# Kernel tuning notes

Hardware: AMD Instinct MI355X
Metric: run time of the kernel (lower is better)

Reference implementation:

```python
import jax, jax.numpy as jnp
import numpy as np

EMBED = 512
HEADS = 8
INTER = 512
HEAD_DIM = INTER // HEADS
ROPE_BASE = 10000.0


def rot_half(x):
    x1 = x[..., ::2]
    x2 = x[..., 1::2]
    return jnp.stack([-x2, x1], axis=-1).reshape(x.shape)


def apply_rope(x, cos, sin):
    # cos/sin: (1, T, 1, 1, D//2) -> repeat-interleave to D
    cos = jnp.repeat(cos, 2, axis=-1)
    sin = jnp.repeat(sin, 2, axis=-1)
    return x * cos + rot_half(x) * sin


def setup_inputs() -> dict:
    key = jax.random.key(0)
    ks = jax.random.split(key, 8)
    B, T, P, E = 2, 512, 16, EMBED
    s_in = 1.0 / np.sqrt(E)
    x = jax.random.normal(ks[0], (B, T, P, E), dtype=jnp.float32)
    q_w = jax.random.normal(ks[1], (INTER, E), dtype=jnp.float32) * s_in
    k_w = jax.random.normal(ks[2], (INTER, E), dtype=jnp.float32) * s_in
    v_w = jax.random.normal(ks[3], (INTER, E), dtype=jnp.float32) * s_in
    q_b = jax.random.normal(ks[4], (INTER,), dtype=jnp.float32) * 0.01
    k_b = jax.random.normal(ks[5], (INTER,), dtype=jnp.float32) * 0.01
    v_b = jax.random.normal(ks[6], (INTER,), dtype=jnp.float32) * 0.01
    proj_w = jax.random.normal(ks[7], (E, INTER), dtype=jnp.float32) * (1.0 / np.sqrt(INTER))
    return {"x": x, "q_w": q_w, "q_b": q_b, "k_w": k_w, "k_b": k_b,
            "v_w": v_w, "v_b": v_b, "proj_w": proj_w}


def reference(x, q_w, q_b, k_w, k_b, v_w, v_b, proj_w):
    B, T, P, E = x.shape
    H, D = HEADS, HEAD_DIM
    q = (x @ q_w.T + q_b).reshape(B, T, P, H, D)
    k = (x @ k_w.T + k_b).reshape(B, T, P, H, D)
    v = (x @ v_w.T + v_b).reshape(B, T, P, H, D)
    # RoPE cache over time axis
    inv_freq = 1.0 / (ROPE_BASE ** (jnp.arange(0, D, 2, dtype=jnp.float32) / D))
    freqs = jnp.arange(T, dtype=jnp.float32)[:, None] * inv_freq[None, :]  # (T, D//2)
    cos_t = jnp.cos(freqs).reshape(1, T, 1, 1, D // 2)
    sin_t = jnp.sin(freqs).reshape(1, T, 1, 1, D // 2)
    q = apply_rope(q, cos_t, sin_t)
    k = apply_rope(k, cos_t, sin_t)
    scale = D ** (-0.5)
    scores = jnp.einsum('btphd,buphd->bphtu', q, k) * scale  # (B,P,H,T,T)
    causal_mask = jnp.triu(jnp.ones((T, T), dtype=bool), k=1)
    scores = jnp.where(causal_mask, -jnp.inf, scores)
    probs = jax.nn.softmax(scores, axis=-1)
    y = jnp.einsum('bphtu,buphd->btphd', probs, v).reshape(B, T, P, H * D)
    return y @ proj_w.T
```

## Files before the change

kernel.cpp:

```cpp
#include <hip/hip_runtime.h>
#include <hip/hip_bf16.h>
#include <math.h>

typedef __bf16 bf16x8 __attribute__((ext_vector_type(8)));
typedef float f32x4 __attribute__((ext_vector_type(4)));
typedef unsigned short u16;

#define MROWS 16384
#define TT 512
#define PP 16

__device__ __forceinline__ u16 f2bf(float f) {
    union { float f; unsigned int i; } v; v.f = f;
    unsigned int x = v.i;
    return (u16)((x + 0x7FFFu + ((x >> 16) & 1u)) >> 16);
}

__device__ __forceinline__ void async16(const u16* g, u16* lds) {
    __builtin_amdgcn_global_load_lds(
        (const __attribute__((address_space(1))) void*)g,
        (__attribute__((address_space(3))) void*)lds, 16, 0, 0);
}

__global__ __launch_bounds__(256) void cvt_k(const float* __restrict__ s,
                                             u16* __restrict__ d) {
    long i = (long)blockIdx.x * 256 + threadIdx.x;
    const float4* p = (const float4*)s + i * 2;
    float4 a = p[0], b = p[1];
    u16 t[8] = { f2bf(a.x), f2bf(a.y), f2bf(a.z), f2bf(a.w),
                 f2bf(b.x), f2bf(b.y), f2bf(b.z), f2bf(b.w) };
    *(uint4*)(d + i * 8) = *(const uint4*)t;
}

__global__ __launch_bounds__(256) void cvtw_k(const float* __restrict__ q,
                                              const float* __restrict__ k,
                                              const float* __restrict__ v,
                                              const float* __restrict__ pw,
                                              u16* __restrict__ d) {
    int m = blockIdx.y;
    const float* s = (m == 0) ? q : (m == 1) ? k : (m == 2) ? v : pw;
    long i = (long)blockIdx.x * 256 + threadIdx.x;
    const float4* p = (const float4*)s + i * 2;
    float4 a = p[0], b = p[1];
    u16 t[8] = { f2bf(a.x), f2bf(a.y), f2bf(a.z), f2bf(a.w),
                 f2bf(b.x), f2bf(b.y), f2bf(b.z), f2bf(b.w) };
    *(uint4*)(d + (long)m * 262144 + i * 8) = *(const uint4*)t;
}

template<bool QKV>
__global__ __launch_bounds__(256, 2)
void gemm_k(const u16* __restrict__ A, const u16* __restrict__ Wall,
            const float* __restrict__ bq, const float* __restrict__ bk,
            const float* __restrict__ bv,
            u16* __restrict__ Oq, u16* __restrict__ Ok, u16* __restrict__ Ov,
            float* __restrict__ Of)
{
    __shared__ u16 As[128 * 64];
    __shared__ u16 Bs[128 * 64];

    const int tid  = threadIdx.x;
    const int wv   = tid >> 6;
    const int lane = tid & 63;
    const int quad = lane >> 4;
    const int l16  = lane & 15;
    const int wm   = wv >> 1, wn = wv & 1;

    const int blockM = blockIdx.x;
    const int blockN = blockIdx.y;

    const u16* W; const float* bias; u16* OutB; int ncol0; int section = 0;
    if constexpr (QKV) {
        section = blockN >> 2;
        ncol0 = (blockN & 3) * 128;
        W    = Wall + (long)section * 262144;
        bias = (section == 0) ? bq : (section == 1) ? bk : bv;
        OutB = (section == 0) ? Oq : (section == 1) ? Ok : Ov;
    } else {
        ncol0 = blockN * 128;
        W = Wall; bias = nullptr; OutB = nullptr;
    }

    const int gm0 = blockM * 128;
    const int lr  = lane >> 3;
    const int lc  = (lane & 7) ^ lr;

    f32x4 acc[4][4] = {};

    for (int kk = 0; kk < 8; ++kk) {
        const int k0 = kk * 64;
        __syncthreads();
        #pragma unroll
        for (int i = 0; i < 4; ++i) {
            const int rb = wv * 32 + i * 8;
            async16(&A[(long)(gm0   + rb + lr) * 512 + k0 + lc * 8], &As[rb * 64]);
            async16(&W[(long)(ncol0 + rb + lr) * 512 + k0 + lc * 8], &Bs[rb * 64]);
        }
        __syncthreads();

        #pragma unroll
        for (int ks = 0; ks < 2; ++ks) {
            bf16x8 af[4], bf_[4];
            #pragma unroll
            for (int ms = 0; ms < 4; ++ms) {
                const int R = wm * 64 + ms * 16 + l16;
                af[ms] = *(const bf16x8*)&As[(R * 8 + ((ks * 4 + quad) ^ (l16 & 7))) * 8];
            }
            #pragma unroll
            for (int ns = 0; ns < 4; ++ns) {
                const int R = wn * 64 + ns * 16 + l16;
                bf_[ns] = *(const bf16x8*)&Bs[(R * 8 + ((ks * 4 + quad) ^ (l16 & 7))) * 8];
            }
            #pragma unroll
            for (int ms = 0; ms < 4; ++ms)
                #pragma unroll
                for (int ns = 0; ns < 4; ++ns)
                    acc[ms][ns] = __builtin_amdgcn_mfma_f32_16x16x32_bf16(af[ms], bf_[ns], acc[ms][ns], 0, 0, 0);
        }
    }

    #pragma unroll
    for (int ms = 0; ms < 4; ++ms) {
        const int g_m0 = gm0 + wm * 64 + ms * 16 + quad * 4;
        #pragma unroll
        for (int ns = 0; ns < 4; ++ns) {
            const int n_local = ncol0 + wn * 64 + ns * 16 + l16;
            float bval = 0.f;
            if constexpr (QKV) bval = bias[n_local];
            #pragma unroll
            for (int r = 0; r < 4; ++r) {
                float val = acc[ms][ns][r] + bval;
                const size_t off = (size_t)(g_m0 + r) * 512 + n_local;
                if constexpr (QKV) {
                    float partner = __shfl_xor(val, 1, 64);
                    if (section < 2) {
                        const int m = g_m0 + r;
                        const int t = (m >> 4) & 511;
                        const int d = n_local & 63;
                        float ang = (float)t * __expf(-(float)(d & ~1) * (9.210340371976184f / 64.0f));
                        float s_, c_;
                        __sincosf(ang, &s_, &c_);
                        val = (d & 1) ? (val * c_ + partner * s_)
                                      : (val * c_ - partner * s_);
                    }
                    OutB[off] = f2bf(val);
                } else {
                    Of[off] = val;
                }
            }
        }
    }
}

__global__ __launch_bounds__(256, 4)
void attn_k(const u16* __restrict__ Q, const u16* __restrict__ K,
            const u16* __restrict__ V, u16* __restrict__ Y)
{
    __shared__ u16 Sh[64 * 64];
    __shared__ u16 Vt[64][72];

    const int tid  = threadIdx.x;
    const int wv   = tid >> 6;
    const int lane = tid & 63;
    const int quad = lane >> 4;
    const int l16  = lane & 15;
    const int lr   = lane >> 3;
    const int lc   = (lane & 7) ^ lr;

    const int pairx = blockIdx.x;
    const int hid = blockIdx.y;
    const int b = hid >> 7;
    const int p = (hid >> 3) & 15;
    const int h = hid & 7;

    const int base = ((b * TT) * PP + p) * 512 + h * 64;
    const int rowStride = PP * 512;

    for (int sel = 0; sel < 2; ++sel) {
        const int qt = sel ? (7 - pairx) : pairx;
        const int t0 = qt * 64;

        __syncthreads();
        #pragma unroll
        for (int i = 0; i < 2; ++i) {
            const int rb = wv * 16 + i * 8;
            async16(&Q[base + (t0 + rb + lr) * rowStride + lc * 8], &Sh[rb * 64]);
        }
        __syncthreads();
        bf16x8 qf[2];
        {
            const int R = wv * 16 + l16;
            #pragma unroll
            for (int ks = 0; ks < 2; ++ks)
                qf[ks] = *(const bf16x8*)&Sh[(R * 8 + ((ks * 4 + quad) ^ (l16 & 7))) * 8];
        }

        float m_i[4], l_i[4], alpha[4];
        f32x4 o[4] = {};
        #pragma unroll
        for (int j = 0; j < 4; ++j) { m_i[j] = -3.0e38f; l_i[j] = 0.f; }

        for (int ui = 0; ui <= qt; ++ui) {
            const int u0 = ui * 64;
            __syncthreads();
            #pragma unroll
            for (int i = 0; i < 2; ++i) {
                const int rb = wv * 16 + i * 8;
                async16(&K[base + (u0 + rb + lr) * rowStride + lc * 8], &Sh[rb * 64]);
            }
            #pragma unroll
            for (int i = 0; i < 4; ++i) {
                int task = tid + i * 256;
                int u = task >> 4, dc = (task & 15) * 4;
                uint2 vvv = *(const uint2*)&V[base + (u0 + u) * rowStride + dc];
                Vt[dc + 0][u] = (u16)(vvv.x & 0xFFFF);
                Vt[dc + 1][u] = (u16)(vvv.x >> 16);
                Vt[dc + 2][u] = (u16)(vvv.y & 0xFFFF);
                Vt[dc + 3][u] = (u16)(vvv.y >> 16);
            }
            __syncthreads();

            f32x4 s[4] = {};
            #pragma unroll
            for (int ks = 0; ks < 2; ++ks) {
                bf16x8 bk_[4];
                #pragma unroll
                for (int ns = 0; ns < 4; ++ns) {
                    const int R = ns * 16 + l16;
                    bk_[ns] = *(const bf16x8*)&Sh[(R * 8 + ((ks * 4 + quad) ^ (l16 & 7))) * 8];
                }
                #pragma unroll
                for (int ns = 0; ns < 4; ++ns)
                    s[ns] = __builtin_amdgcn_mfma_f32_16x16x32_bf16(qf[ks], bk_[ns], s[ns], 0, 0, 0);
            }
            __syncthreads();

            if (ui == qt) {
                #pragma unroll
                for (int ns = 0; ns < 4; ++ns)
                    #pragma unroll
                    for (int r = 0; r < 4; ++r) {
                        int trow = wv * 16 + quad * 4 + r;
                        int ucol = ns * 16 + l16;
                        float v = s[ns][r] * 0.125f;
                        s[ns][r] = (ucol > trow) ? -1.0e30f : v;
                    }
            } else {
                #pragma unroll
                for (int ns = 0; ns < 4; ++ns)
                    #pragma unroll
                    for (int r = 0; r < 4; ++r)
                        s[ns][r] *= 0.125f;
            }
            #pragma unroll
            for (int r = 0; r < 4; ++r) {
                float tmax = s[0][r];
                #pragma unroll
                for (int ns = 1; ns < 4; ++ns) tmax = fmaxf(tmax, s[ns][r]);
                #pragma unroll
                for (int off = 1; off < 16; off <<= 1)
                    tmax = fmaxf(tmax, __shfl_xor(tmax, off, 64));
                float mn = fmaxf(m_i[r], tmax);
                alpha[r] = __expf(fminf(m_i[r] - mn, 0.f));
                m_i[r] = mn;
                float rsum = 0.f;
                #pragma unroll
                for (int ns = 0; ns < 4; ++ns) {
                    float e = __expf(fminf(s[ns][r] - mn, 0.f));
                    s[ns][r] = e;
                    rsum += e;
                }
                #pragma unroll
                for (int off = 1; off < 16; off <<= 1)
                    rsum += __shfl_xor(rsum, off, 64);
                l_i[r] = l_i[r] * alpha[r] + rsum;
            }
            #pragma unroll
            for (int nd = 0; nd < 4; ++nd)
                #pragma unroll
                for (int r = 0; r < 4; ++r)
                    o[nd][r] *= alpha[r];
            #pragma unroll
            for (int ns = 0; ns < 4; ++ns)
                #pragma unroll
                for (int r = 0; r < 4; ++r) {
                    const int row = wv * 16 + quad * 4 + r;
                    const int cu  = ns * 2 + (l16 >> 3);
                    Sh[(row * 8 + (cu ^ (row & 7))) * 8 + (l16 & 7)] = f2bf(s[ns][r]);
                }
            __syncthreads();
            #pragma unroll
            for (int ks = 0; ks < 2; ++ks) {
                const int R = wv * 16 + l16;
                bf16x8 ap = *(const bf16x8*)&Sh[(R * 8 + ((ks * 4 + quad) ^ (l16 & 7))) * 8];
                bf16x8 bv_[4];
                #pragma unroll
                for (int nd = 0; nd < 4; ++nd)
                    bv_[nd] = *(const bf16x8*)&Vt[nd * 16 + l16][ks * 32 + quad * 8];
                #pragma unroll
                for (int nd = 0; nd < 4; ++nd)
                    o[nd] = __builtin_amdgcn_mfma_f32_16x16x32_bf16(ap, bv_[nd], o[nd], 0, 0, 0);
            }
        }

        #pragma unroll
        for (int nd = 0; nd < 4; ++nd)
            #pragma unroll
            for (int r = 0; r < 4; ++r) {
                int t = t0 + wv * 16 + quad * 4 + r;
                int d = nd * 16 + l16;
                float val = o[nd][r] / l_i[r];
                int ym = (b * TT + t) * PP + p;
                Y[ym * 512 + h * 64 + d] = f2bf(val);
            }
    }
}

extern "C" void kernel_launch(void* const* d_in, const int* in_sizes, int n_in,
                              void* d_out, int out_size, void* d_ws, size_t ws_size,
                              hipStream_t stream) {
    const float* x  = (const float*)d_in[0];
    const float* qw = (const float*)d_in[1];
    const float* qb = (const float*)d_in[2];
    const float* kw = (const float*)d_in[3];
    const float* kb = (const float*)d_in[4];
    const float* vw = (const float*)d_in[5];
    const float* vb = (const float*)d_in[6];
    const float* pw = (const float*)d_in[7];

    u16* ws   = (u16*)d_ws;
    u16* xb   = ws;
    u16* wAll = ws + (size_t)MROWS * 512;
    u16* Qb   = wAll + 4 * 262144;
    u16* Vb   = (u16*)d_out;
    u16* Kb   = (u16*)d_out + (size_t)MROWS * 512;

    cvt_k<<<4096, 256, 0, stream>>>(x, xb);
    cvtw_k<<<dim3(128, 4), 256, 0, stream>>>(qw, kw, vw, pw, wAll);
    gemm_k<true><<<dim3(128, 12), 256, 0, stream>>>(xb, wAll, qb, kb, vb,
                                                    Qb, Kb, Vb, nullptr);
    attn_k<<<dim3(4, 256), 256, 0, stream>>>(Qb, Kb, Vb, Qb);
    gemm_k<false><<<dim3(128, 4), 256, 0, stream>>>(Qb, wAll + 3 * 262144,
                                                    nullptr, nullptr, nullptr,
                                                    nullptr, nullptr, nullptr,
                                                    (float*)d_out);
}
```

Measured before the change: 195.9 us.

## Pre-transpose V, fold softmax scale into Q, compute row sums via MFMA

Adds a separate kernel that writes V transposed per head plane, so attention can async-load V tiles into swizzled LDS. The block no longer transposes V in LDS every iteration. The softmax scale and log2e are folded into Q at the projection epilogue so exp2f can be used directly. Row sums are accumulated with an extra MFMA against a ones vector instead of shuffle reductions. Blocks now handle one query tile each, with separate K, V and P LDS buffers and higher occupancy. The cost is an extra kernel launch and a round trip through global memory.

```diff
diff --git a/kernel.cpp b/kernel.cpp
--- a/kernel.cpp
+++ b/kernel.cpp
@@ -141,6 +141,7 @@
                         __sincosf(ang, &s_, &c_);
                         val = (d & 1) ? (val * c_ + partner * s_)
                                       : (val * c_ - partner * s_);
+                        if (section == 0) val *= 0.18033688011112042f;
                     }
                     OutB[off] = f2bf(val);
                 } else {
@@ -151,12 +152,41 @@
     }
 }
 
-__global__ __launch_bounds__(256, 4)
+__global__ __launch_bounds__(256) void tv_k(const u16* __restrict__ Vb,
+                                            u16* __restrict__ Vtg) {
+    __shared__ u16 Vs[64][72];
+    const int tid = threadIdx.x;
+    const int ut = blockIdx.x, plane = blockIdx.y;
+    const int b = plane >> 7, p = (plane >> 3) & 15, h = plane & 7;
+    const int base = ((b * TT) * PP + p) * 512 + h * 64;
+    const int u0 = ut * 64;
+    #pragma unroll
+    for (int i = 0; i < 4; ++i) {
+        int task = tid + i * 256;
+        int u = task >> 4, dc = (task & 15) * 4;
+        uint2 vv = *(const uint2*)&Vb[base + (u0 + u) * 8192 + dc];
+        Vs[dc + 0][u] = (u16)(vv.x & 0xFFFF);
+        Vs[dc + 1][u] = (u16)(vv.x >> 16);
+        Vs[dc + 2][u] = (u16)(vv.y & 0xFFFF);
+        Vs[dc + 3][u] = (u16)(vv.y >> 16);
+    }
+    __syncthreads();
+    #pragma unroll
+    for (int i = 0; i < 2; ++i) {
+        int task = tid + i * 256;
+        int d = task >> 3, uc = (task & 7) * 8;
+        *(uint4*)&Vtg[(size_t)plane * 32768 + d * 512 + u0 + uc] =
+            *(const uint4*)&Vs[d][uc];
+    }
+}
+
+__global__ __launch_bounds__(256, 6)
 void attn_k(const u16* __restrict__ Q, const u16* __restrict__ K,
-            const u16* __restrict__ V, u16* __restrict__ Y)
+            const u16* __restrict__ Vtg, u16* __restrict__ Y)
 {
-    __shared__ u16 Sh[64 * 64];
-    __shared__ u16 Vt[64][72];
+    __shared__ u16 ShK[64 * 64];
+    __shared__ u16 ShV[64 * 64];
+    __shared__ u16 ShP[64 * 64];
 
     const int tid  = threadIdx.x;
     const int wv   = tid >> 6;
@@ -166,7 +196,8 @@
     const int lr   = lane >> 3;
     const int lc   = (lane & 7) ^ lr;
 
-    const int pairx = blockIdx.x;
+    const int qt  = 7 - blockIdx.x;
+    const int t0  = qt * 64;
     const int hid = blockIdx.y;
     const int b = hid >> 7;
     const int p = (hid >> 3) & 15;
@@ -174,145 +205,125 @@
 
     const int base = ((b * TT) * PP + p) * 512 + h * 64;
     const int rowStride = PP * 512;
-
-    for (int sel = 0; sel < 2; ++sel) {
-        const int qt = sel ? (7 - pairx) : pairx;
-        const int t0 = qt * 64;
-
+    const size_t planeOff = (size_t)hid * 32768;
+
+    #pragma unroll
+    for (int i = 0; i < 2; ++i) {
+        const int rb = wv * 16 + i * 8;
+        async16(&Q[base + (t0 + rb + lr) * rowStride + lc * 8], &ShK[rb * 64]);
+    }
+    __syncthreads();
+    bf16x8 qf[2];
+    {
+        const int R = wv * 16 + l16;
+        #pragma unroll
+        for (int ks = 0; ks < 2; ++ks)
+            qf[ks] = *(const bf16x8*)&ShK[(R * 8 + ((ks * 4 + quad) ^ (l16 & 7))) * 8];
+    }
+
+    bf16x8 ones;
+    #pragma unroll
+    for (int j = 0; j < 8; ++j) ones[j] = (__bf16)1.0f;
+
+    float m_i[4], alpha[4];
+    f32x4 o[4] = {};
+    f32x4 ol = {};
+    #pragma unroll
+    for (int j = 0; j < 4; ++j) m_i[j] = -3.0e38f;
+
+    for (int ui = 0; ui <= qt; ++ui) {
+        const int u0 = ui * 64;
         __syncthreads();
         #pragma unroll
         for (int i = 0; i < 2; ++i) {
             const int rb = wv * 16 + i * 8;
-            async16(&Q[base + (t0 + rb + lr) * rowStride + lc * 8], &Sh[rb * 64]);
-        }
-        __syncthreads();
-        bf16x8 qf[2];
-        {
-            const int R = wv * 16 + l16;
-            #pragma unroll
-            for (int ks = 0; ks < 2; ++ks)
-                qf[ks] = *(const bf16x8*)&Sh[(R * 8 + ((ks * 4 + quad) ^ (l16 & 7))) * 8];
-        }
-
-        float m_i[4], l_i[4], alpha[4];
-        f32x4 o[4] = {};
-        #pragma unroll
-        for (int j = 0; j < 4; ++j) { m_i[j] = -3.0e38f; l_i[j] = 0.f; }
-
-        for (int ui = 0; ui <= qt; ++ui) {
-            const int u0 = ui * 64;
-            __syncthreads();
-            #pragma unroll
-            for (int i = 0; i < 2; ++i) {
-                const int rb = wv * 16 + i * 8;
-                async16(&K[base + (u0 + rb + lr) * rowStride + lc * 8], &Sh[rb * 64]);
-            }
-            #pragma unroll
-            for (int i = 0; i < 4; ++i) {
-                int task = tid + i * 256;
-                int u = task >> 4, dc = (task & 15) * 4;
-                uint2 vvv = *(const uint2*)&V[base + (u0 + u) * rowStride + dc];
-                Vt[dc + 0][u] = (u16)(vvv.x & 0xFFFF);
-                Vt[dc + 1][u] = (u16)(vvv.x >> 16);
-                Vt[dc + 2][u] = (u16)(vvv.y & 0xFFFF);
-                Vt[dc + 3][u] = (u16)(vvv.y >> 16);
-            }
-            __syncthreads();
-
-            f32x4 s[4] = {};
-            #pragma unroll
-            for (int ks = 0; ks < 2; ++ks) {
-                bf16x8 bk_[4];
-                #pragma unroll
-                for (int ns = 0; ns < 4; ++ns) {
-                    const int R = ns * 16 + l16;
-                    bk_[ns] = *(const bf16x8*)&Sh[(R * 8 + ((ks * 4 + quad) ^ (l16 & 7))) * 8];
-                }
-                #pragma unroll
-                for (int ns = 0; ns < 4; ++ns)
-                    s[ns] = __builtin_amdgcn_mfma_f32_16x16x32_bf16(qf[ks], bk_[ns], s[ns], 0, 0, 0);
-            }
-            __syncthreads();
-
-            if (ui == qt) {
-                #pragma unroll
-                for (int ns = 0; ns < 4; ++ns)
-                    #pragma unroll
-                    for (int r = 0; r < 4; ++r) {
-                        int trow = wv * 16 + quad * 4 + r;
-                        int ucol = ns * 16 + l16;
-                        float v = s[ns][r] * 0.125f;
-                        s[ns][r] = (ucol > trow) ? -1.0e30f : v;
-                    }
-            } else {
-                #pragma unroll
-                for (int ns = 0; ns < 4; ++ns)
-                    #pragma unroll
-                    for (int r = 0; r < 4; ++r)
-                        s[ns][r] *= 0.125f;
-            }
-            #pragma unroll
-            for (int r = 0; r < 4; ++r) {
-                float tmax = s[0][r];
-                #pragma unroll
-                for (int ns = 1; ns < 4; ++ns) tmax = fmaxf(tmax, s[ns][r]);
-                #pragma unroll
-                for (int off = 1; off < 16; off <<= 1)
-                    tmax = fmaxf(tmax, __shfl_xor(tmax, off, 64));
-                float mn = fmaxf(m_i[r], tmax);
-                alpha[r] = __expf(fminf(m_i[r] - mn, 0.f));
-                m_i[r] = mn;
-                float rsum = 0.f;
-                #pragma unroll
-                for (int ns = 0; ns < 4; ++ns) {
-                    float e = __expf(fminf(s[ns][r] - mn, 0.f));
-                    s[ns][r] = e;
-                    rsum += e;
-                }
-                #pragma unroll
-                for (int off = 1; off < 16; off <<= 1)
-                    rsum += __shfl_xor(rsum, off, 64);
-                l_i[r] = l_i[r] * alpha[r] + rsum;
-            }
-            #pragma unroll
-            for (int nd = 0; nd < 4; ++nd)
-                #pragma unroll
-                for (int r = 0; r < 4; ++r)
-                    o[nd][r] *= alpha[r];
+            async16(&K[base + (u0 + rb + lr) * rowStride + lc * 8], &ShK[rb * 64]);
+            async16(&Vtg[planeOff + (rb + lr) * 512 + u0 + lc * 8], &ShV[rb * 64]);
+        }
+        __syncthreads();
+
+        f32x4 s[4] = {};
+        #pragma unroll
+        for (int ks = 0; ks < 2; ++ks) {
+            bf16x8 bk_[4];
+            #pragma unroll
+            for (int ns = 0; ns < 4; ++ns) {
+                const int R = ns * 16 + l16;
+                bk_[ns] = *(const bf16x8*)&ShK[(R * 8 + ((ks * 4 + quad) ^ (l16 & 7))) * 8];
+            }
+            #pragma unroll
+            for (int ns = 0; ns < 4; ++ns)
+                s[ns] = __builtin_amdgcn_mfma_f32_16x16x32_bf16(qf[ks], bk_[ns], s[ns], 0, 0, 0);
+        }
+
+        if (ui == qt) {
             #pragma unroll
             for (int ns = 0; ns < 4; ++ns)
                 #pragma unroll
                 for (int r = 0; r < 4; ++r) {
-                    const int row = wv * 16 + quad * 4 + r;
-                    const int cu  = ns * 2 + (l16 >> 3);
-                    Sh[(row * 8 + (cu ^ (row & 7))) * 8 + (l16 & 7)] = f2bf(s[ns][r]);
+                    int trow = wv * 16 + quad * 4 + r;
+                    int ucol = ns * 16 + l16;
+                    if (ucol > trow) s[ns][r] = -1.0e30f;
                 }
-            __syncthreads();
-            #pragma unroll
-            for (int ks = 0; ks < 2; ++ks) {
-                const int R = wv * 16 + l16;
-                bf16x8 ap = *(const bf16x8*)&Sh[(R * 8 + ((ks * 4 + quad) ^ (l16 & 7))) * 8];
-                bf16x8 bv_[4];
-                #pragma unroll
-                for (int nd = 0; nd < 4; ++nd)
-                    bv_[nd] = *(const bf16x8*)&Vt[nd * 16 + l16][ks * 32 + quad * 8];
-                #pragma unroll
-                for (int nd = 0; nd < 4; ++nd)
-                    o[nd] = __builtin_amdgcn_mfma_f32_16x16x32_bf16(ap, bv_[nd], o[nd], 0, 0, 0);
-            }
-        }
-
+        }
+        #pragma unroll
+        for (int r = 0; r < 4; ++r) {
+            float tmax = s[0][r];
+            #pragma unroll
+            for (int ns = 1; ns < 4; ++ns) tmax = fmaxf(tmax, s[ns][r]);
+            #pragma unroll
+            for (int off = 1; off < 16; off <<= 1)
+                tmax = fmaxf(tmax, __shfl_xor(tmax, off, 64));
+            float mn = fmaxf(m_i[r], tmax);
+            alpha[r] = exp2f(fminf(m_i[r] - mn, 0.f));
+            m_i[r] = mn;
+            #pragma unroll
+            for (int ns = 0; ns < 4; ++ns)
+                s[ns][r] = exp2f(fminf(s[ns][r] - mn, 0.f));
+        }
         #pragma unroll
         for (int nd = 0; nd < 4; ++nd)
             #pragma unroll
+            for (int r = 0; r < 4; ++r)
+                o[nd][r] *= alpha[r];
+        #pragma unroll
+        for (int r = 0; r < 4; ++r) ol[r] *= alpha[r];
+        #pragma unroll
+        for (int ns = 0; ns < 4; ++ns)
+            #pragma unroll
             for (int r = 0; r < 4; ++r) {
-                int t = t0 + wv * 16 + quad * 4 + r;
-                int d = nd * 16 + l16;
-                float val = o[nd][r] / l_i[r];
-                int ym = (b * TT + t) * PP + p;
-                Y[ym * 512 + h * 64 + d] = f2bf(val);
-            }
-    }
+                const int row = wv * 16 + quad * 4 + r;
+                const int cu  = ns * 2 + (l16 >> 3);
+                ShP[(row * 8 + (cu ^ (row & 7))) * 8 + (l16 & 7)] = f2bf(s[ns][r]);
+            }
+        __syncthreads();
+        #pragma unroll
+        for (int ks = 0; ks < 2; ++ks) {
+            const int R = wv * 16 + l16;
+            bf16x8 ap = *(const bf16x8*)&ShP[(R * 8 + ((ks * 4 + quad) ^ (l16 & 7))) * 8];
+            bf16x8 bv_[4];
+            #pragma unroll
+            for (int nd = 0; nd < 4; ++nd) {
+                const int R4 = nd * 16 + l16;
+                bv_[nd] = *(const bf16x8*)&ShV[(R4 * 8 + ((ks * 4 + quad) ^ (l16 & 7))) * 8];
+            }
+            #pragma unroll
+            for (int nd = 0; nd < 4; ++nd)
+                o[nd] = __builtin_amdgcn_mfma_f32_16x16x32_bf16(ap, bv_[nd], o[nd], 0, 0, 0);
+            ol = __builtin_amdgcn_mfma_f32_16x16x32_bf16(ap, ones, ol, 0, 0, 0);
+        }
+    }
+
+    #pragma unroll
+    for (int nd = 0; nd < 4; ++nd)
+        #pragma unroll
+        for (int r = 0; r < 4; ++r) {
+            int t = t0 + wv * 16 + quad * 4 + r;
+            int d = nd * 16 + l16;
+            float val = o[nd][r] / ol[r];
+            int ym = (b * TT + t) * PP + p;
+            Y[ym * 512 + h * 64 + d] = f2bf(val);
+        }
 }
 
 extern "C" void kernel_launch(void* const* d_in, const int* in_sizes, int n_in,
@@ -333,12 +344,14 @@
     u16* Qb   = wAll + 4 * 262144;
     u16* Vb   = (u16*)d_out;
     u16* Kb   = (u16*)d_out + (size_t)MROWS * 512;
+    u16* Vtg  = xb;
 
     cvt_k<<<4096, 256, 0, stream>>>(x, xb);
     cvtw_k<<<dim3(128, 4), 256, 0, stream>>>(qw, kw, vw, pw, wAll);
     gemm_k<true><<<dim3(128, 12), 256, 0, stream>>>(xb, wAll, qb, kb, vb,
                                                     Qb, Kb, Vb, nullptr);
-    attn_k<<<dim3(4, 256), 256, 0, stream>>>(Qb, Kb, Vb, Qb);
+    tv_k<<<dim3(8, 256), 256, 0, stream>>>(Vb, Vtg);
+    attn_k<<<dim3(8, 256), 256, 0, stream>>>(Qb, Kb, Vtg, Qb);
     gemm_k<false><<<dim3(128, 4), 256, 0, stream>>>(Qb, wAll + 3 * 262144,
                                                     nullptr, nullptr, nullptr,
                                                     nullptr, nullptr, nullptr,
```

Measured after the change: 262.0 us. +33.7%, slower.

## Fold softmax scale into Q, use exp2, compute row sums via MFMA, merge convert kernels

Applied to the files above, without the earlier changes.

Merges the two fp32-to-bf16 conversion kernels into one launch. Pre-multiplies Q by scale·log2(e) in the QKV GEMM epilogue so attention can drop the per-score scaling and use exp2 directly. Replaces the shuffle-based row-sum reduction with an extra MFMA against a ones vector, accumulating the softmax denominator from the bf16 probabilities. The denominator now comes from bf16-rounded probabilities, which slightly changes numerics but matches the numerator's rounding.

```diff
diff --git a/kernel.cpp b/kernel.cpp
--- a/kernel.cpp
+++ b/kernel.cpp
@@ -22,29 +22,26 @@
         (__attribute__((address_space(3))) void*)lds, 16, 0, 0);
 }
 
-__global__ __launch_bounds__(256) void cvt_k(const float* __restrict__ s,
-                                             u16* __restrict__ d) {
-    long i = (long)blockIdx.x * 256 + threadIdx.x;
-    const float4* p = (const float4*)s + i * 2;
+__global__ __launch_bounds__(256) void cvtall_k(const float* __restrict__ x,
+                                                const float* __restrict__ qw,
+                                                const float* __restrict__ kw,
+                                                const float* __restrict__ vw,
+                                                const float* __restrict__ pw,
+                                                u16* __restrict__ d) {
+    long c = (long)blockIdx.x * 256 + threadIdx.x;
+    const float* s; long off;
+    if (c < 1048576) { s = x; off = c; }
+    else {
+        long j = c - 1048576;
+        int m = (int)(j >> 15);
+        s = (m == 0) ? qw : (m == 1) ? kw : (m == 2) ? vw : pw;
+        off = j & 32767;
+    }
+    const float4* p = (const float4*)s + off * 2;
     float4 a = p[0], b = p[1];
     u16 t[8] = { f2bf(a.x), f2bf(a.y), f2bf(a.z), f2bf(a.w),
                  f2bf(b.x), f2bf(b.y), f2bf(b.z), f2bf(b.w) };
-    *(uint4*)(d + i * 8) = *(const uint4*)t;
-}
-
-__global__ __launch_bounds__(256) void cvtw_k(const float* __restrict__ q,
-                                              const float* __restrict__ k,
-                                              const float* __restrict__ v,
-                                              const float* __restrict__ pw,
-                                              u16* __restrict__ d) {
-    int m = blockIdx.y;
-    const float* s = (m == 0) ? q : (m == 1) ? k : (m == 2) ? v : pw;
-    long i = (long)blockIdx.x * 256 + threadIdx.x;
-    const float4* p = (const float4*)s + i * 2;
-    float4 a = p[0], b = p[1];
-    u16 t[8] = { f2bf(a.x), f2bf(a.y), f2bf(a.z), f2bf(a.w),
-                 f2bf(b.x), f2bf(b.y), f2bf(b.z), f2bf(b.w) };
-    *(uint4*)(d + (long)m * 262144 + i * 8) = *(const uint4*)t;
+    *(uint4*)(d + c * 8) = *(const uint4*)t;
 }
 
 template<bool QKV>
@@ -141,6 +138,7 @@
                         __sincosf(ang, &s_, &c_);
                         val = (d & 1) ? (val * c_ + partner * s_)
                                       : (val * c_ - partner * s_);
+                        if (section == 0) val *= 0.18033688011112042f;
                     }
                     OutB[off] = f2bf(val);
                 } else {
@@ -175,6 +173,10 @@
     const int base = ((b * TT) * PP + p) * 512 + h * 64;
     const int rowStride = PP * 512;
 
+    bf16x8 ones;
+    #pragma unroll
+    for (int j = 0; j < 8; ++j) ones[j] = (__bf16)1.0f;
+
     for (int sel = 0; sel < 2; ++sel) {
         const int qt = sel ? (7 - pairx) : pairx;
         const int t0 = qt * 64;
@@ -194,10 +196,11 @@
                 qf[ks] = *(const bf16x8*)&Sh[(R * 8 + ((ks * 4 + quad) ^ (l16 & 7))) * 8];
         }
 
-        float m_i[4], l_i[4], alpha[4];
+        float m_i[4], alpha[4];
         f32x4 o[4] = {};
-        #pragma unroll
-        for (int j = 0; j < 4; ++j) { m_i[j] = -3.0e38f; l_i[j] = 0.f; }
+        f32x4 ol = {};
+        #pragma unroll
+        for (int j = 0; j < 4; ++j) m_i[j] = -3.0e38f;
 
         for (int ui = 0; ui <= qt; ++ui) {
             const int u0 = ui * 64;
@@ -241,15 +244,8 @@
                     for (int r = 0; r < 4; ++r) {
                         int trow = wv * 16 + quad * 4 + r;
                         int ucol = ns * 16 + l16;
-                        float v = s[ns][r] * 0.125f;
-                        s[ns][r] = (ucol > trow) ? -1.0e30f : v;
+                        if (ucol > trow) s[ns][r] = -1.0e30f;
                     }
-            } else {
-                #pragma unroll
-                for (int ns = 0; ns < 4; ++ns)
-                    #pragma unroll
-                    for (int r = 0; r < 4; ++r)
-                        s[ns][r] *= 0.125f;
             }
             #pragma unroll
             for (int r = 0; r < 4; ++r) {
@@ -260,25 +256,19 @@
                 for (int off = 1; off < 16; off <<= 1)
                     tmax = fmaxf(tmax, __shfl_xor(tmax, off, 64));
                 float mn = fmaxf(m_i[r], tmax);
-                alpha[r] = __expf(fminf(m_i[r] - mn, 0.f));
+                alpha[r] = exp2f(fminf(m_i[r] - mn, 0.f));
                 m_i[r] = mn;
-                float rsum = 0.f;
-                #pragma unroll
-                for (int ns = 0; ns < 4; ++ns) {
-                    float e = __expf(fminf(s[ns][r] - mn, 0.f));
-                    s[ns][r] = e;
-                    rsum += e;
-                }
-                #pragma unroll
-                for (int off = 1; off < 16; off <<= 1)
-                    rsum += __shfl_xor(rsum, off, 64);
-                l_i[r] = l_i[r] * alpha[r] + rsum;
+                #pragma unroll
+                for (int ns = 0; ns < 4; ++ns)
+                    s[ns][r] = exp2f(fminf(s[ns][r] - mn, 0.f));
             }
             #pragma unroll
             for (int nd = 0; nd < 4; ++nd)
                 #pragma unroll
                 for (int r = 0; r < 4; ++r)
                     o[nd][r] *= alpha[r];
+            #pragma unroll
+            for (int r = 0; r < 4; ++r) ol[r] *= alpha[r];
             #pragma unroll
             for (int ns = 0; ns < 4; ++ns)
                 #pragma unroll
@@ -299,6 +289,7 @@
                 #pragma unroll
                 for (int nd = 0; nd < 4; ++nd)
                     o[nd] = __builtin_amdgcn_mfma_f32_16x16x32_bf16(ap, bv_[nd], o[nd], 0, 0, 0);
+                ol = __builtin_amdgcn_mfma_f32_16x16x32_bf16(ap, ones, ol, 0, 0, 0);
             }
         }
 
@@ -308,7 +299,7 @@
             for (int r = 0; r < 4; ++r) {
                 int t = t0 + wv * 16 + quad * 4 + r;
                 int d = nd * 16 + l16;
-                float val = o[nd][r] / l_i[r];
+                float val = o[nd][r] / ol[r];
                 int ym = (b * TT + t) * PP + p;
                 Y[ym * 512 + h * 64 + d] = f2bf(val);
             }
@@ -334,8 +325,7 @@
     u16* Vb   = (u16*)d_out;
     u16* Kb   = (u16*)d_out + (size_t)MROWS * 512;
 
-    cvt_k<<<4096, 256, 0, stream>>>(x, xb);
-    cvtw_k<<<dim3(128, 4), 256, 0, stream>>>(qw, kw, vw, pw, wAll);
+    cvtall_k<<<4608, 256, 0, stream>>>(x, qw, kw, vw, pw, xb);
     gemm_k<true><<<dim3(128, 12), 256, 0, stream>>>(xb, wAll, qb, kb, vb,
                                                     Qb, Kb, Vb, nullptr);
     attn_k<<<dim3(4, 256), 256, 0, stream>>>(Qb, Kb, Vb, Qb);
```

Result: faster. 189.6 us (-3.2%).
